# Optimization experiments

Hardware: AMD Instinct MI355X
Metric: run time of the kernel (lower is better)

The kernel has to match this reference:

```python
import jax, jax.numpy as jnp
import numpy as np

HEADS = 8
KS = 7
PAD = 3


def grouped_conv1x1(x, w):
    # x: (B, Cin, H, W), w: (heads, Cout/h, Cin/h) -> (B, Cout, H, W)
    B, Cin, H, W = x.shape
    g, co, ci = w.shape
    xg = x.reshape(B, g, ci, H, W)
    out = jnp.einsum('bgchw,goc->bgohw', xg, w)
    return out.reshape(B, g * co, H, W)


def unfold2d(p, k):
    # p: (B, C, Hp, Wp) -> (B, C, H, W, k, k) sliding windows, stride 1
    B, C, Hp, Wp = p.shape
    H, W = Hp - k + 1, Wp - k + 1
    rows = [jnp.stack([p[:, :, i:i + H, j:j + W] for j in range(k)], axis=-1)
            for i in range(k)]
    return jnp.stack(rows, axis=-2)  # (B,C,H,W,k,k)


def setup_inputs() -> dict:
    key = jax.random.key(0)
    ks = jax.random.split(key, 7)
    B, Cin, H, W = 8, 64, 64, 64
    Cout = 64
    g = HEADS
    return {
        'x': jax.random.normal(ks[0], (B, Cin, H, W), jnp.float32),
        'r': jax.random.normal(ks[1], (1,), jnp.float32),
        'w_q': jax.random.normal(ks[2], (g, Cout // g, Cin // g), jnp.float32) * 0.2,
        'w_k': jax.random.normal(ks[3], (g, Cout // g, Cin // g), jnp.float32) * 0.2,
        'w_v': jax.random.normal(ks[4], (g, Cout // g, Cin // g), jnp.float32) * 0.2,
        'rel_h': jax.random.normal(ks[5], (Cout // 2, KS), jnp.float32),
        'rel_w': jax.random.normal(ks[6], (Cout // 2, KS), jnp.float32),
    }


def reference(x, r, w_q, w_k, w_v, rel_h, rel_w):
    B, Cin, H, W = x.shape
    g = HEADS
    Cout = w_q.shape[0] * w_q.shape[1]
    dh = Cout // g

    padded = jnp.pad(x, ((0, 0), (0, 0), (PAD, PAD), (PAD, PAD)))
    q = grouped_conv1x1(x, w_q)            # (B, Cout, H, W)
    k = grouped_conv1x1(padded, w_k)       # (B, Cout, H+2p, W+2p)
    v = grouped_conv1x1(padded, w_v)

    k = unfold2d(k, KS)                    # (B, Cout, H, W, KS, KS)
    v = unfold2d(v, KS)

    # learnable relative positional encoding: split channels in half,
    # add rel_h along window-height, rel_w along window-width
    half = Cout // 2
    k_h = k[:, :half] + rel_h[None, :, None, None, :, None]
    k_w = k[:, half:] + rel_w[None, :, None, None, None, :]
    k = jnp.concatenate([k_h, k_w], axis=1)

    K2 = KS * KS
    k = k.reshape(B, g, dh, H, W, K2)
    v = v.reshape(B, g, dh, H, W, K2)
    q = q.reshape(B, g, dh, H, W, 1)

    scale = np.sqrt(g / Cout).astype(np.float32)
    logits = (q * k).sum(axis=2, keepdims=True) * scale   # (B,g,1,H,W,K2)
    attn = jax.nn.softmax(logits, axis=-1)
    out = (attn * v).sum(axis=-1)                          # (B,g,dh,H,W)
    return out.reshape(B, Cout, H, W)
```

## Files before the change

### kernel.cpp

```cpp
#include <hip/hip_runtime.h>
#include <math.h>

#define NG  8
#define DH  8
#define NCP 4
#define KS  7
#define PAD 3
#define TH  16
#define TW  32
#define OW  2
#define TPH 22
#define RSTW 40
#define PLW  (TPH * RSTW)
#define CH  64
#define HH  64
#define WW  64

typedef __fp16 h2v __attribute__((ext_vector_type(2)));
typedef __fp16 h4v __attribute__((ext_vector_type(4)));
typedef __fp16 h8v __attribute__((ext_vector_type(8)));

#if __has_builtin(__builtin_amdgcn_exp2f)
#define EXP2(x) __builtin_amdgcn_exp2f(x)
#else
#define EXP2(x) exp2f(x)
#endif

__device__ __forceinline__ int imin(int a, int b) { return a < b ? a : b; }
__device__ __forceinline__ int imax(int a, int b) { return a > b ? a : b; }

__global__ __launch_bounds__(256, 2)
void saconv_kernel(const float* __restrict__ x,
                   const float* __restrict__ wq,
                   const float* __restrict__ wk,
                   const float* __restrict__ wv,
                   const float* __restrict__ relh,
                   const float* __restrict__ relw,
                   float* __restrict__ out) {
  __shared__ h2v xs2[NCP * PLW];
  __shared__ h2v swq2[DH * NCP];
  __shared__ h2v swv2[DH * NCP];
  __shared__ h2v swk2[DH * NCP];
  __shared__ h2v srel2[KS * NCP];

  const int tx  = threadIdx.x;
  const int ty  = threadIdx.y;
  const int tid = ty * 16 + tx;
  const int bz  = blockIdx.z;
  const int b   = bz >> 3;
  const int g   = bz & 7;
  const int h0  = blockIdx.y * TH;
  const int w0  = blockIdx.x * TW;

  const float sl2e = 0.35355339059327373f * 1.4426950408889634f;

  if (tid < 32) {
    int c = tid >> 2, cp = tid & 3;
    swq2[tid] = __builtin_amdgcn_cvt_pkrtz(wq[g * 64 + c * 8 + 2 * cp],
                                           wq[g * 64 + c * 8 + 2 * cp + 1]);
  } else if (tid < 64) {
    int t2 = tid - 32;
    int c = t2 >> 2, cp = t2 & 3;
    swv2[t2] = __builtin_amdgcn_cvt_pkrtz(wv[g * 64 + c * 8 + 2 * cp],
                                          wv[g * 64 + c * 8 + 2 * cp + 1]);
  } else if (tid < 96) {
    int t2 = tid - 64;
    int ci = t2 >> 2, cP = t2 & 3;
    swk2[t2] = __builtin_amdgcn_cvt_pkrtz(wk[g * 64 + (2 * cP) * 8 + ci] * sl2e,
                                          wk[g * 64 + (2 * cP + 1) * 8 + ci] * sl2e);
  } else if (tid < 96 + KS * NCP) {
    int t2 = tid - 96;
    int t = t2 >> 2, cP = t2 & 3;
    float a0, a1;
    if (g < 4) {
      a0 = relh[(g * 8 + 2 * cP) * KS + t];
      a1 = relh[(g * 8 + 2 * cP + 1) * KS + t];
    } else {
      a0 = relw[((g - 4) * 8 + 2 * cP) * KS + t];
      a1 = relw[((g - 4) * 8 + 2 * cP + 1) * KS + t];
    }
    srel2[t2] = __builtin_amdgcn_cvt_pkrtz(a0 * sl2e, a1 * sl2e);
  }

  const float* xb = x + (size_t)(b * CH + g * DH) * (HH * WW);
  if (tid < 176) {
    const int half = tid / 88;
    const int rem  = tid - half * 88;
    const int pair = rem / 22;
    const int row  = rem - pair * 22;
    const int yy   = h0 + row - PAD;
    const bool yok = (yy >= 0) & (yy < HH);
    const int  cy  = imin(imax(yy, 0), HH - 1);
    const float* pl0 = xb + ((size_t)(2 * pair) * HH + cy) * WW;
    const float* pl1 = pl0 + HH * WW;

    float4 qa[6], qb[6];
    #pragma unroll
    for (int u = 0; u < 6; u++) {
      int qc = w0 - 4 + 4 * (5 * half + u);
      bool qin = yok & (qc >= 0) & (qc <= WW - 4);
      int qs = qin ? qc : 0;
      float4 A = *(const float4*)(pl0 + qs);
      float4 B = *(const float4*)(pl1 + qs);
      float4 Z = make_float4(0.f, 0.f, 0.f, 0.f);
      qa[u] = qin ? A : Z;
      qb[u] = qin ? B : Z;
    }
    #pragma unroll
    for (int c = 0; c < 5; c++) {
      h2v e0 = __builtin_amdgcn_cvt_pkrtz(qa[c].y, qb[c].y);
      h2v e1 = __builtin_amdgcn_cvt_pkrtz(qa[c].z, qb[c].z);
      h2v e2 = __builtin_amdgcn_cvt_pkrtz(qa[c].w, qb[c].w);
      h2v e3 = __builtin_amdgcn_cvt_pkrtz(qa[c + 1].x, qb[c + 1].x);
      h8v w8 = { e0.x, e0.y, e1.x, e1.y, e2.x, e2.y, e3.x, e3.y };
      *(h8v*)&xs2[pair * PLW + row * RSTW + 4 * (5 * half + c)] = w8;
    }
  }
  __syncthreads();

  h2v  qkh[OW][NCP];
  float rq[OW][KS];
  {
    h2v xc2[OW][NCP];
    #pragma unroll
    for (int o = 0; o < OW; o++)
      #pragma unroll
      for (int cp = 0; cp < NCP; cp++)
        xc2[o][cp] = xs2[cp * PLW + (ty + PAD) * RSTW + (2 * tx + o + PAD)];

    #pragma unroll
    for (int o = 0; o < OW; o++) {
      float q_[DH];
      #pragma unroll
      for (int c = 0; c < DH; c++) {
        float a = 0.f;
        #pragma unroll
        for (int cp = 0; cp < NCP; cp++)
          a = __builtin_amdgcn_fdot2(swq2[c * 4 + cp], xc2[o][cp], a, false);
        q_[c] = a;
      }
      h2v qp[NCP];
      #pragma unroll
      for (int cP = 0; cP < NCP; cP++)
        qp[cP] = __builtin_amdgcn_cvt_pkrtz(q_[2 * cP], q_[2 * cP + 1]);

      float qkt[DH];
      #pragma unroll
      for (int ci = 0; ci < DH; ci++) {
        float a = 0.f;
        #pragma unroll
        for (int cP = 0; cP < NCP; cP++)
          a = __builtin_amdgcn_fdot2(qp[cP], swk2[ci * 4 + cP], a, false);
        qkt[ci] = a;
      }
      #pragma unroll
      for (int cp = 0; cp < NCP; cp++)
        qkh[o][cp] = __builtin_amdgcn_cvt_pkrtz(qkt[2 * cp], qkt[2 * cp + 1]);

      #pragma unroll
      for (int t = 0; t < KS; t++) {
        float a = 0.f;
        #pragma unroll
        for (int cP = 0; cP < NCP; cP++)
          a = __builtin_amdgcn_fdot2(qp[cP], srel2[t * 4 + cP], a, false);
        rq[o][t] = a;
      }
    }
  }

  float s[OW], xa[OW][DH];
  #pragma unroll
  for (int o = 0; o < OW; o++) {
    s[o] = 0.f;
    #pragma unroll
    for (int ci = 0; ci < DH; ci++) xa[o][ci] = 0.f;
  }

#define WINLOOP(DINIT)                                                         \
  _Pragma("unroll")                                                            \
  for (int i = 0; i < KS; i++) {                                               \
    const int wbase = (ty + i) * RSTW + 2 * tx;                                \
    h2v xw[NCP][8];                                                            \
    _Pragma("unroll")                                                          \
    for (int cp = 0; cp < NCP; cp++) {                                         \
      const h4v* bp = (const h4v*)&xs2[cp * PLW + wbase];                      \
      h4v r0 = bp[0], r1 = bp[1], r2 = bp[2], r3 = bp[3];                      \
      xw[cp][0] = __builtin_shufflevector(r0, r0, 0, 1);                       \
      xw[cp][1] = __builtin_shufflevector(r0, r0, 2, 3);                       \
      xw[cp][2] = __builtin_shufflevector(r1, r1, 0, 1);                       \
      xw[cp][3] = __builtin_shufflevector(r1, r1, 2, 3);                       \
      xw[cp][4] = __builtin_shufflevector(r2, r2, 0, 1);                       \
      xw[cp][5] = __builtin_shufflevector(r2, r2, 2, 3);                       \
      xw[cp][6] = __builtin_shufflevector(r3, r3, 0, 1);                       \
      xw[cp][7] = __builtin_shufflevector(r3, r3, 2, 3);                       \
    }                                                                          \
    _Pragma("unroll")                                                          \
    for (int o = 0; o < OW; o++) {                                             \
      float e[KS];                                                             \
      float se = 0.f;                                                          \
      _Pragma("unroll")                                                        \
      for (int j = 0; j < KS; j++) {                                           \
        float d = (DINIT);                                                     \
        _Pragma("unroll")                                                      \
        for (int cp = 0; cp < NCP; cp++)                                       \
          d = __builtin_amdgcn_fdot2(qkh[o][cp], xw[cp][o + j], d, false);     \
        e[j] = EXP2(d);                                                        \
        se += e[j];                                                            \
      }                                                                        \
      s[o] += se;                                                              \
      _Pragma("unroll")                                                        \
      for (int cp = 0; cp < NCP; cp++) {                                       \
        float a0 = xa[o][2 * cp];                                              \
        float a1 = xa[o][2 * cp + 1];                                          \
        _Pragma("unroll")                                                      \
        for (int j = 0; j < KS; j++) {                                         \
          a0 = fmaf(e[j], (float)xw[cp][o + j].x, a0);                         \
          a1 = fmaf(e[j], (float)xw[cp][o + j].y, a1);                         \
        }                                                                      \
        xa[o][2 * cp]     = a0;                                                \
        xa[o][2 * cp + 1] = a1;                                                \
      }                                                                        \
    }                                                                          \
  }

  if (g < 4) { WINLOOP(rq[o][i]) }
  else       { WINLOOP(rq[o][j]) }
#undef WINLOOP

  h2v xav2[OW][NCP];
  #pragma unroll
  for (int o = 0; o < OW; o++) {
    float inv = 1.0f / s[o];
    #pragma unroll
    for (int cp = 0; cp < NCP; cp++)
      xav2[o][cp] = __builtin_amdgcn_cvt_pkrtz(xa[o][2 * cp] * inv,
                                               xa[o][2 * cp + 1] * inv);
  }

  const int h = h0 + ty;
  const int wbase = w0 + 2 * tx;
  #pragma unroll
  for (int c = 0; c < DH; c++) {
    float a0 = 0.f, a1 = 0.f;
    #pragma unroll
    for (int cp = 0; cp < NCP; cp++) {
      a0 = __builtin_amdgcn_fdot2(swv2[c * 4 + cp], xav2[0][cp], a0, false);
      a1 = __builtin_amdgcn_fdot2(swv2[c * 4 + cp], xav2[1][cp], a1, false);
    }
    *(float2*)(&out[((size_t)(b * CH + g * DH + c) * HH + h) * WW + wbase]) =
        make_float2(a0, a1);
  }
}

extern "C" void kernel_launch(void* const* d_in, const int* in_sizes, int n_in,
                              void* d_out, int out_size, void* d_ws, size_t ws_size,
                              hipStream_t stream) {
  const float* x    = (const float*)d_in[0];
  const float* wq   = (const float*)d_in[2];
  const float* wk   = (const float*)d_in[3];
  const float* wv   = (const float*)d_in[4];
  const float* relh = (const float*)d_in[5];
  const float* relw = (const float*)d_in[6];
  float* out = (float*)d_out;

  const int B = in_sizes[0] / (CH * HH * WW);
  dim3 grid(WW / TW, HH / TH, B * NG);
  dim3 block(16, 16, 1);
  saconv_kernel<<<grid, block, 0, stream>>>(x, wq, wk, wv, relh, relw, out);
}
```

Measured before the change: 18.13 us.

## Widen tile to full image row and restructure halo staging into LDS

The tile width grows from 32 to the full 64-column row and blocks grow to 512 threads, so horizontal halo columns are no longer loaded twice across neighbouring blocks. The global-to-LDS staging is rewritten: each thread loads 16 contiguous floats per channel pair with no column bounds checks, and a separate group of threads zero-fills the left and right padding columns. This cuts redundant halo traffic and per-load predication. In exchange the grid has half as many blocks (256), which may lower occupancy on a GPU with many CUs, and the larger blocks put more pressure on registers.

```diff
diff --git a/kernel.cpp b/kernel.cpp
--- a/kernel.cpp
+++ b/kernel.cpp
@@ -7,10 +7,10 @@
 #define KS  7
 #define PAD 3
 #define TH  16
-#define TW  32
+#define TW  64
 #define OW  2
 #define TPH 22
-#define RSTW 40
+#define RSTW 72
 #define PLW  (TPH * RSTW)
 #define CH  64
 #define HH  64
@@ -18,7 +18,6 @@
 
 typedef __fp16 h2v __attribute__((ext_vector_type(2)));
 typedef __fp16 h4v __attribute__((ext_vector_type(4)));
-typedef __fp16 h8v __attribute__((ext_vector_type(8)));
 
 #if __has_builtin(__builtin_amdgcn_exp2f)
 #define EXP2(x) __builtin_amdgcn_exp2f(x)
@@ -29,7 +28,7 @@
 __device__ __forceinline__ int imin(int a, int b) { return a < b ? a : b; }
 __device__ __forceinline__ int imax(int a, int b) { return a > b ? a : b; }
 
-__global__ __launch_bounds__(256, 2)
+__global__ __launch_bounds__(512, 2)
 void saconv_kernel(const float* __restrict__ x,
                    const float* __restrict__ wq,
                    const float* __restrict__ wk,
@@ -45,12 +44,11 @@
 
   const int tx  = threadIdx.x;
   const int ty  = threadIdx.y;
-  const int tid = ty * 16 + tx;
-  const int bz  = blockIdx.z;
+  const int tid = ty * 32 + tx;
+  const int bz  = blockIdx.y;
   const int b   = bz >> 3;
   const int g   = bz & 7;
-  const int h0  = blockIdx.y * TH;
-  const int w0  = blockIdx.x * TW;
+  const int h0  = blockIdx.x * TH;
 
   const float sl2e = 0.35355339059327373f * 1.4426950408889634f;
 
@@ -83,38 +81,49 @@
   }
 
   const float* xb = x + (size_t)(b * CH + g * DH) * (HH * WW);
-  if (tid < 176) {
-    const int half = tid / 88;
-    const int rem  = tid - half * 88;
-    const int pair = rem / 22;
-    const int row  = rem - pair * 22;
-    const int yy   = h0 + row - PAD;
+  if (tid < 352) {
+    const int cp  = tid / 88;
+    const int rem = tid - cp * 88;
+    const int row = rem >> 2;
+    const int q   = rem & 3;
+    const int yy  = h0 + row - PAD;
     const bool yok = (yy >= 0) & (yy < HH);
-    const int  cy  = imin(imax(yy, 0), HH - 1);
-    const float* pl0 = xb + ((size_t)(2 * pair) * HH + cy) * WW;
+    const int cy  = imin(imax(yy, 0), HH - 1);
+    const float* pl0 = xb + ((size_t)(2 * cp) * HH + cy) * WW + 16 * q;
     const float* pl1 = pl0 + HH * WW;
-
-    float4 qa[6], qb[6];
-    #pragma unroll
-    for (int u = 0; u < 6; u++) {
-      int qc = w0 - 4 + 4 * (5 * half + u);
-      bool qin = yok & (qc >= 0) & (qc <= WW - 4);
-      int qs = qin ? qc : 0;
-      float4 A = *(const float4*)(pl0 + qs);
-      float4 B = *(const float4*)(pl1 + qs);
-      float4 Z = make_float4(0.f, 0.f, 0.f, 0.f);
-      qa[u] = qin ? A : Z;
-      qb[u] = qin ? B : Z;
-    }
-    #pragma unroll
-    for (int c = 0; c < 5; c++) {
-      h2v e0 = __builtin_amdgcn_cvt_pkrtz(qa[c].y, qb[c].y);
-      h2v e1 = __builtin_amdgcn_cvt_pkrtz(qa[c].z, qb[c].z);
-      h2v e2 = __builtin_amdgcn_cvt_pkrtz(qa[c].w, qb[c].w);
-      h2v e3 = __builtin_amdgcn_cvt_pkrtz(qa[c + 1].x, qb[c + 1].x);
-      h8v w8 = { e0.x, e0.y, e1.x, e1.y, e2.x, e2.y, e3.x, e3.y };
-      *(h8v*)&xs2[pair * PLW + row * RSTW + 4 * (5 * half + c)] = w8;
-    }
+    const float4 Z = make_float4(0.f, 0.f, 0.f, 0.f);
+    float f0[16], f1[16];
+    #pragma unroll
+    for (int u = 0; u < 4; u++) {
+      float4 A = *(const float4*)(pl0 + 4 * u);
+      float4 B = *(const float4*)(pl1 + 4 * u);
+      A = yok ? A : Z;
+      B = yok ? B : Z;
+      f0[4 * u] = A.x; f0[4 * u + 1] = A.y; f0[4 * u + 2] = A.z; f0[4 * u + 3] = A.w;
+      f1[4 * u] = B.x; f1[4 * u + 1] = B.y; f1[4 * u + 2] = B.z; f1[4 * u + 3] = B.w;
+    }
+    h2v* base = &xs2[cp * PLW + row * RSTW + 16 * q];
+    base[3] = __builtin_amdgcn_cvt_pkrtz(f0[0], f1[0]);
+    #pragma unroll
+    for (int k = 0; k < 7; k++) {
+      h2v lo = __builtin_amdgcn_cvt_pkrtz(f0[1 + 2 * k], f1[1 + 2 * k]);
+      h2v hi = __builtin_amdgcn_cvt_pkrtz(f0[2 + 2 * k], f1[2 + 2 * k]);
+      h4v w4 = { lo.x, lo.y, hi.x, hi.y };
+      *(h4v*)&base[4 + 2 * k] = w4;
+    }
+    base[18] = __builtin_amdgcn_cvt_pkrtz(f0[15], f1[15]);
+  } else if (tid < 440) {
+    const int t2  = tid - 352;
+    const int cp  = t2 / 22;
+    const int row = t2 - cp * 22;
+    h2v* base = &xs2[cp * PLW + row * RSTW];
+    const __fp16 z = (__fp16)0.f;
+    h2v z2 = { z, z };
+    h4v z4 = { z, z, z, z };
+    *(h4v*)&base[0] = z4;
+    base[2]  = z2;
+    base[67] = z2;
+    *(h4v*)&base[68] = z4;
   }
   __syncthreads();
 
@@ -238,7 +247,7 @@
   }
 
   const int h = h0 + ty;
-  const int wbase = w0 + 2 * tx;
+  const int wbase = 2 * tx;
   #pragma unroll
   for (int c = 0; c < DH; c++) {
     float a0 = 0.f, a1 = 0.f;
@@ -264,7 +273,7 @@
   float* out = (float*)d_out;
 
   const int B = in_sizes[0] / (CH * HH * WW);
-  dim3 grid(WW / TW, HH / TH, B * NG);
-  dim3 block(16, 16, 1);
+  dim3 grid(HH / TH, B * NG, 1);
+  dim3 block(32, 16, 1);
   saconv_kernel<<<grid, block, 0, stream>>>(x, wq, wk, wv, relh, relw, out);
 }
```

Result: slower. 19.16 us (+5.7%).

## Process two width tiles per block with double-buffered LDS prefetch

Applied to the files above, without the earlier changes.

Each block now covers both 32-wide column tiles of a 16-row strip instead of one. The second tile's global loads are issued before computing the first tile and are written into a second LDS buffer afterwards, so load latency overlaps compute. This halves the grid to 256 blocks and drops launch_bounds to one block per SM. It also moves compute into a noinline function, which risks fewer resident waves and call overhead.

```diff
diff --git a/kernel.cpp b/kernel.cpp
--- a/kernel.cpp
+++ b/kernel.cpp
@@ -7,7 +7,6 @@
 #define KS  7
 #define PAD 3
 #define TH  16
-#define TW  32
 #define OW  2
 #define TPH 22
 #define RSTW 40
@@ -29,95 +28,45 @@
 __device__ __forceinline__ int imin(int a, int b) { return a < b ? a : b; }
 __device__ __forceinline__ int imax(int a, int b) { return a > b ? a : b; }
 
-__global__ __launch_bounds__(256, 2)
-void saconv_kernel(const float* __restrict__ x,
-                   const float* __restrict__ wq,
-                   const float* __restrict__ wk,
-                   const float* __restrict__ wv,
-                   const float* __restrict__ relh,
-                   const float* __restrict__ relw,
-                   float* __restrict__ out) {
-  __shared__ h2v xs2[NCP * PLW];
-  __shared__ h2v swq2[DH * NCP];
-  __shared__ h2v swv2[DH * NCP];
-  __shared__ h2v swk2[DH * NCP];
-  __shared__ h2v srel2[KS * NCP];
-
-  const int tx  = threadIdx.x;
-  const int ty  = threadIdx.y;
-  const int tid = ty * 16 + tx;
-  const int bz  = blockIdx.z;
-  const int b   = bz >> 3;
-  const int g   = bz & 7;
-  const int h0  = blockIdx.y * TH;
-  const int w0  = blockIdx.x * TW;
-
-  const float sl2e = 0.35355339059327373f * 1.4426950408889634f;
-
-  if (tid < 32) {
-    int c = tid >> 2, cp = tid & 3;
-    swq2[tid] = __builtin_amdgcn_cvt_pkrtz(wq[g * 64 + c * 8 + 2 * cp],
-                                           wq[g * 64 + c * 8 + 2 * cp + 1]);
-  } else if (tid < 64) {
-    int t2 = tid - 32;
-    int c = t2 >> 2, cp = t2 & 3;
-    swv2[t2] = __builtin_amdgcn_cvt_pkrtz(wv[g * 64 + c * 8 + 2 * cp],
-                                          wv[g * 64 + c * 8 + 2 * cp + 1]);
-  } else if (tid < 96) {
-    int t2 = tid - 64;
-    int ci = t2 >> 2, cP = t2 & 3;
-    swk2[t2] = __builtin_amdgcn_cvt_pkrtz(wk[g * 64 + (2 * cP) * 8 + ci] * sl2e,
-                                          wk[g * 64 + (2 * cP + 1) * 8 + ci] * sl2e);
-  } else if (tid < 96 + KS * NCP) {
-    int t2 = tid - 96;
-    int t = t2 >> 2, cP = t2 & 3;
-    float a0, a1;
-    if (g < 4) {
-      a0 = relh[(g * 8 + 2 * cP) * KS + t];
-      a1 = relh[(g * 8 + 2 * cP + 1) * KS + t];
-    } else {
-      a0 = relw[((g - 4) * 8 + 2 * cP) * KS + t];
-      a1 = relw[((g - 4) * 8 + 2 * cP + 1) * KS + t];
-    }
-    srel2[t2] = __builtin_amdgcn_cvt_pkrtz(a0 * sl2e, a1 * sl2e);
-  }
-
-  const float* xb = x + (size_t)(b * CH + g * DH) * (HH * WW);
-  if (tid < 176) {
-    const int half = tid / 88;
-    const int rem  = tid - half * 88;
-    const int pair = rem / 22;
-    const int row  = rem - pair * 22;
-    const int yy   = h0 + row - PAD;
-    const bool yok = (yy >= 0) & (yy < HH);
-    const int  cy  = imin(imax(yy, 0), HH - 1);
-    const float* pl0 = xb + ((size_t)(2 * pair) * HH + cy) * WW;
-    const float* pl1 = pl0 + HH * WW;
-
-    float4 qa[6], qb[6];
-    #pragma unroll
-    for (int u = 0; u < 6; u++) {
-      int qc = w0 - 4 + 4 * (5 * half + u);
-      bool qin = yok & (qc >= 0) & (qc <= WW - 4);
-      int qs = qin ? qc : 0;
-      float4 A = *(const float4*)(pl0 + qs);
-      float4 B = *(const float4*)(pl1 + qs);
-      float4 Z = make_float4(0.f, 0.f, 0.f, 0.f);
-      qa[u] = qin ? A : Z;
-      qb[u] = qin ? B : Z;
-    }
-    #pragma unroll
-    for (int c = 0; c < 5; c++) {
-      h2v e0 = __builtin_amdgcn_cvt_pkrtz(qa[c].y, qb[c].y);
-      h2v e1 = __builtin_amdgcn_cvt_pkrtz(qa[c].z, qb[c].z);
-      h2v e2 = __builtin_amdgcn_cvt_pkrtz(qa[c].w, qb[c].w);
-      h2v e3 = __builtin_amdgcn_cvt_pkrtz(qa[c + 1].x, qb[c + 1].x);
-      h8v w8 = { e0.x, e0.y, e1.x, e1.y, e2.x, e2.y, e3.x, e3.y };
-      *(h8v*)&xs2[pair * PLW + row * RSTW + 4 * (5 * half + c)] = w8;
-    }
-  }
-  __syncthreads();
-
+__device__ __forceinline__ void stage_load(const float* xb, int hb, int w0,
+                                           int half, int pair, int row,
+                                           float4* qa, float4* qb) {
+  const int yy  = hb + row - PAD;
+  const bool yok = (yy >= 0) & (yy < HH);
+  const int  cy  = imin(imax(yy, 0), HH - 1);
+  const float* pl0 = xb + ((size_t)(2 * pair) * HH + cy) * WW;
+  const float* pl1 = pl0 + HH * WW;
+  const float4 Z = make_float4(0.f, 0.f, 0.f, 0.f);
+  #pragma unroll
+  for (int u = 0; u < 6; u++) {
+    int qc = w0 - 4 + 4 * (5 * half + u);
+    bool qin = yok & (qc >= 0) & (qc <= WW - 4);
+    int qs = qin ? qc : 0;
+    float4 A = *(const float4*)(pl0 + qs);
+    float4 B = *(const float4*)(pl1 + qs);
+    qa[u] = qin ? A : Z;
+    qb[u] = qin ? B : Z;
+  }
+}
+
+__device__ __forceinline__ void stage_write(h2v* xsb, int half, int pair, int row,
+                                            const float4* qa, const float4* qb) {
+  #pragma unroll
+  for (int c = 0; c < 5; c++) {
+    h2v e0 = __builtin_amdgcn_cvt_pkrtz(qa[c].y, qb[c].y);
+    h2v e1 = __builtin_amdgcn_cvt_pkrtz(qa[c].z, qb[c].z);
+    h2v e2 = __builtin_amdgcn_cvt_pkrtz(qa[c].w, qb[c].w);
+    h2v e3 = __builtin_amdgcn_cvt_pkrtz(qa[c + 1].x, qb[c + 1].x);
+    h8v w8 = { e0.x, e0.y, e1.x, e1.y, e2.x, e2.y, e3.x, e3.y };
+    *(h8v*)&xsb[pair * PLW + row * RSTW + 4 * (5 * half + c)] = w8;
+  }
+}
+
+__device__ __attribute__((noinline)) void compute_tile(
+    const h2v* xsb, const h2v* swq2, const h2v* swk2,
+    const h2v* srel2, const h2v* swv2,
+    int tx, int ty, int g, int hb, int w0, int b,
+    float* __restrict__ out) {
   h2v  qkh[OW][NCP];
   float rq[OW][KS];
   {
@@ -126,7 +75,7 @@
     for (int o = 0; o < OW; o++)
       #pragma unroll
       for (int cp = 0; cp < NCP; cp++)
-        xc2[o][cp] = xs2[cp * PLW + (ty + PAD) * RSTW + (2 * tx + o + PAD)];
+        xc2[o][cp] = xsb[cp * PLW + (ty + PAD) * RSTW + (2 * tx + o + PAD)];
 
     #pragma unroll
     for (int o = 0; o < OW; o++) {
@@ -183,7 +132,7 @@
     h2v xw[NCP][8];                                                            \
     _Pragma("unroll")                                                          \
     for (int cp = 0; cp < NCP; cp++) {                                         \
-      const h4v* bp = (const h4v*)&xs2[cp * PLW + wbase];                      \
+      const h4v* bp = (const h4v*)&xsb[cp * PLW + wbase];                      \
       h4v r0 = bp[0], r1 = bp[1], r2 = bp[2], r3 = bp[3];                      \
       xw[cp][0] = __builtin_shufflevector(r0, r0, 0, 1);                       \
       xw[cp][1] = __builtin_shufflevector(r0, r0, 2, 3);                       \
@@ -237,8 +186,8 @@
                                                xa[o][2 * cp + 1] * inv);
   }
 
-  const int h = h0 + ty;
-  const int wbase = w0 + 2 * tx;
+  const int h = hb + ty;
+  const int wb = w0 + 2 * tx;
   #pragma unroll
   for (int c = 0; c < DH; c++) {
     float a0 = 0.f, a1 = 0.f;
@@ -247,9 +196,94 @@
       a0 = __builtin_amdgcn_fdot2(swv2[c * 4 + cp], xav2[0][cp], a0, false);
       a1 = __builtin_amdgcn_fdot2(swv2[c * 4 + cp], xav2[1][cp], a1, false);
     }
-    *(float2*)(&out[((size_t)(b * CH + g * DH + c) * HH + h) * WW + wbase]) =
+    *(float2*)(&out[((size_t)(b * CH + g * DH + c) * HH + h) * WW + wb]) =
         make_float2(a0, a1);
   }
+}
+
+__global__ __launch_bounds__(256, 1)
+void saconv_kernel(const float* __restrict__ x,
+                   const float* __restrict__ wq,
+                   const float* __restrict__ wk,
+                   const float* __restrict__ wv,
+                   const float* __restrict__ relh,
+                   const float* __restrict__ relw,
+                   float* __restrict__ out) {
+  __shared__ h2v xs2[2][NCP * PLW];
+  __shared__ h2v swq2[DH * NCP];
+  __shared__ h2v swv2[DH * NCP];
+  __shared__ h2v swk2[DH * NCP];
+  __shared__ h2v srel2[KS * NCP];
+
+  const int tx  = threadIdx.x;
+  const int ty  = threadIdx.y;
+  const int tid = ty * 16 + tx;
+  const int bz  = blockIdx.y;
+  const int b   = bz >> 3;
+  const int g   = bz & 7;
+  const int hb  = blockIdx.x * TH;
+
+  const float sl2e = 0.35355339059327373f * 1.4426950408889634f;
+
+  if (tid < 32) {
+    int c = tid >> 2, cp = tid & 3;
+    swq2[tid] = __builtin_amdgcn_cvt_pkrtz(wq[g * 64 + c * 8 + 2 * cp],
+                                           wq[g * 64 + c * 8 + 2 * cp + 1]);
+  } else if (tid < 64) {
+    int t2 = tid - 32;
+    int c = t2 >> 2, cp = t2 & 3;
+    swv2[t2] = __builtin_amdgcn_cvt_pkrtz(wv[g * 64 + c * 8 + 2 * cp],
+                                          wv[g * 64 + c * 8 + 2 * cp + 1]);
+  } else if (tid < 96) {
+    int t2 = tid - 64;
+    int ci = t2 >> 2, cP = t2 & 3;
+    swk2[t2] = __builtin_amdgcn_cvt_pkrtz(wk[g * 64 + (2 * cP) * 8 + ci] * sl2e,
+                                          wk[g * 64 + (2 * cP + 1) * 8 + ci] * sl2e);
+  } else if (tid < 96 + KS * NCP) {
+    int t2 = tid - 96;
+    int t = t2 >> 2, cP = t2 & 3;
+    float a0, a1;
+    if (g < 4) {
+      a0 = relh[(g * 8 + 2 * cP) * KS + t];
+      a1 = relh[(g * 8 + 2 * cP + 1) * KS + t];
+    } else {
+      a0 = relw[((g - 4) * 8 + 2 * cP) * KS + t];
+      a1 = relw[((g - 4) * 8 + 2 * cP + 1) * KS + t];
+    }
+    srel2[t2] = __builtin_amdgcn_cvt_pkrtz(a0 * sl2e, a1 * sl2e);
+  }
+
+  const float* xb = x + (size_t)(b * CH + g * DH) * (HH * WW);
+  const bool stager = (tid < 176);
+  int half = 0, pair = 0, rowS = 0;
+  if (stager) {
+    half = tid / 88;
+    int rem = tid - half * 88;
+    pair = rem / 22;
+    rowS = rem - pair * 22;
+  }
+
+  {
+    float4 qa[6], qb[6];
+    if (stager) {
+      stage_load(xb, hb, 0, half, pair, rowS, qa, qb);
+      stage_write(&xs2[0][0], half, pair, rowS, qa, qb);
+    }
+  }
+  __syncthreads();
+
+  float4 qa[6], qb[6];
+  if (stager)
+    stage_load(xb, hb, 32, half, pair, rowS, qa, qb);
+  __builtin_amdgcn_sched_barrier(0);
+
+  compute_tile(&xs2[0][0], swq2, swk2, srel2, swv2, tx, ty, g, hb, 0, b, out);
+
+  if (stager)
+    stage_write(&xs2[1][0], half, pair, rowS, qa, qb);
+  __syncthreads();
+
+  compute_tile(&xs2[1][0], swq2, swk2, srel2, swv2, tx, ty, g, hb, 32, b, out);
 }
 
 extern "C" void kernel_launch(void* const* d_in, const int* in_sizes, int n_in,
@@ -264,7 +298,7 @@
   float* out = (float*)d_out;
 
   const int B = in_sizes[0] / (CH * HH * WW);
-  dim3 grid(WW / TW, HH / TH, B * NG);
+  dim3 grid(HH / TH, B * NG, 1);
   dim3 block(16, 16, 1);
   saconv_kernel<<<grid, block, 0, stream>>>(x, wq, wk, wv, relh, relw, out);
 }
```

Result: slower. 20.21 us (+11.4%).
